# Optimization experiments

Measured on AMD Instinct MI355X. Metric: run time of the kernel, lower is better.

The kernel has to match this reference:

```python
import jax, jax.numpy as jnp
import numpy as np

E_ROUTER = 32      # routed experts with real FFNs
ZERO_E = 8         # zero-experts (identity skip)
TOP_K = 4
ROUTED_SCALE = 2.5


def setup_inputs() -> dict:
    key = jax.random.key(0)
    k1, k2, k3, k4, k5 = jax.random.split(key, 5)
    T, H, I = 2048, 1024, 512
    N = E_ROUTER + ZERO_E
    return {
        "hidden_states": jax.random.normal(k1, (T, H), jnp.float32),
        "router_w": jax.random.normal(k2, (N, H), jnp.float32) * 0.02,            # classifier weight [N, H]
        "e_score_correction_bias": jax.random.normal(k3, (N,), jnp.float32) * 0.01,
        "w13": jax.random.normal(k4, (E_ROUTER, 2 * I, H), jnp.float32) * 0.02,   # gate+up per expert
        "w2": jax.random.normal(k5, (E_ROUTER, H, I), jnp.float32) * 0.02,        # down proj per expert
    }


def reference(hidden_states, router_w, e_score_correction_bias, w13, w2):
    T, H = hidden_states.shape
    I = w2.shape[-1]

    # --- router (LongcatFlashTopkRouter) ---
    logits = hidden_states @ router_w.T                         # [T, N]
    scores = jax.nn.softmax(logits, axis=-1)
    biased = scores + e_score_correction_bias[None, :]
    _, topk_ids = jax.lax.top_k(biased, TOP_K)                  # indices chosen on biased scores
    topk_w = jnp.take_along_axis(scores, topk_ids, axis=-1) * ROUTED_SCALE  # weights from unbiased scores

    # --- zero experts: ids >= E_ROUTER contribute weight * x directly ---
    zero_mask = topk_ids >= E_ROUTER
    zero_total = jnp.sum(jnp.where(zero_mask, topk_w, 0.0), axis=-1, keepdims=True)  # [T,1]
    zero_expert_output = hidden_states * zero_total
    topk_w = jnp.where(zero_mask, 0.0, topk_w)
    topk_ids = jnp.where(zero_mask, 0, topk_ids)

    # --- combine weights per (token, expert): scatter-add of topk weights ---
    combine = jnp.zeros((T, E_ROUTER), jnp.float32).at[
        jnp.arange(T)[:, None], topk_ids
    ].add(topk_w)                                               # [T, E]

    # --- experts: swiglu FFN per expert (dense form of grouped GEMM; zero combine
    #     weights make it mathematically identical to dispatch/compute/combine) ---
    gate_up = jnp.einsum('th,eih->eti', hidden_states, w13)     # [E, T, 2I]
    gate, up = gate_up[..., :I], gate_up[..., I:]
    h = jax.nn.silu(gate) * up                                  # [E, T, I]
    expert_out = jnp.einsum('eti,ehi->eth', h, w2)              # [E, T, H]
    routed = jnp.einsum('eth,te->th', expert_out, combine)      # [T, H]

    return routed + zero_expert_output
```

## Files before the change

### kernel.cpp

```cpp
#include <hip/hip_runtime.h>
#include <math.h>

#define TT 2048
#define HH 1024
#define NE 40
#define ER 32
#define II 512
#define TOPK 4
#define RSCALE 2.5f
#define MAXW 96

typedef __bf16 bf16x8 __attribute__((ext_vector_type(8)));
typedef float f32x4 __attribute__((ext_vector_type(4)));

__global__ __launch_bounds__(256) void k_logits(const float* __restrict__ hidden,
                                                const float* __restrict__ rw,
                                                float* __restrict__ logits,
                                                int* __restrict__ cnt,
                                                int* __restrict__ cursor) {
  int tid = threadIdx.x;
  if (blockIdx.x == 0 && tid < 32) { cnt[tid] = 0; cursor[tid] = 0; }
  int lane = tid & 63;
  int t = blockIdx.x * 4 + (tid >> 6);
  const float* hrow = hidden + (size_t)t * HH;
  float4 hv[4];
  #pragma unroll
  for (int c = 0; c < 4; c++)
    hv[c] = *(const float4*)(hrow + c * 256 + lane * 4);
  float mylg = 0.f;
  for (int e = 0; e < NE; e++) {
    const float* wrow = rw + (size_t)e * HH;
    float p = 0.f;
    #pragma unroll
    for (int c = 0; c < 4; c++) {
      float4 wv = *(const float4*)(wrow + c * 256 + lane * 4);
      p += hv[c].x * wv.x + hv[c].y * wv.y + hv[c].z * wv.z + hv[c].w * wv.w;
    }
    #pragma unroll
    for (int off = 32; off; off >>= 1) p += __shfl_xor(p, off);
    if (lane == e) mylg = p;
  }
  if (lane < NE) logits[(size_t)t * NE + lane] = mylg;
}

__global__ __launch_bounds__(256) void k_route(const float* __restrict__ logits,
                                               const float* __restrict__ bias,
                                               const float* __restrict__ hidden,
                                               float* __restrict__ out,
                                               int* __restrict__ cnt,
                                               int* __restrict__ tok4_id,
                                               float* __restrict__ tok4_w,
                                               __bf16* __restrict__ hid_bf) {
  int lane = threadIdx.x & 63;
  int t = blockIdx.x * 4 + (threadIdx.x >> 6);
  float lg = (lane < NE) ? logits[(size_t)t * NE + lane] : -INFINITY;
  float m = lg;
  #pragma unroll
  for (int off = 32; off; off >>= 1) m = fmaxf(m, __shfl_xor(m, off));
  float p = (lane < NE) ? expf(lg - m) : 0.f;
  float s = p;
  #pragma unroll
  for (int off = 32; off; off >>= 1) s += __shfl_xor(s, off);
  float score = p / s;
  float v = (lane < NE) ? score + bias[lane] : -INFINITY;
  int ids[TOPK]; float wv[TOPK];
  #pragma unroll
  for (int k = 0; k < TOPK; k++) {
    float mv = v;
    int mi = (lane < NE) ? lane : 63;
    #pragma unroll
    for (int off = 32; off; off >>= 1) {
      float ov = __shfl_xor(mv, off);
      int oi = __shfl_xor(mi, off);
      if (ov > mv || (ov == mv && oi < mi)) { mv = ov; mi = oi; }
    }
    ids[k] = mi;
    wv[k] = RSCALE * __shfl(score, mi);
    if (lane == mi) v = -INFINITY;
  }
  float zt = 0.f;
  #pragma unroll
  for (int k = 0; k < TOPK; k++) if (ids[k] >= ER) zt += wv[k];
  if (lane == 0) {
    #pragma unroll
    for (int k = 0; k < TOPK; k++) {
      tok4_id[t * TOPK + k] = ids[k];
      tok4_w[t * TOPK + k] = wv[k];
      if (ids[k] < ER) atomicAdd(&cnt[ids[k]], 1);
    }
  }
  #pragma unroll
  for (int c = 0; c < 4; c++) {
    int j = c * 256 + lane * 4;
    float4 h4 = *(const float4*)(hidden + (size_t)t * HH + j);
    float4 o4 = make_float4(h4.x * zt, h4.y * zt, h4.z * zt, h4.w * zt);
    *(float4*)(out + (size_t)t * HH + j) = o4;
    union { __bf16 h[4]; uint2 u; } pk;
    pk.h[0] = (__bf16)h4.x; pk.h[1] = (__bf16)h4.y;
    pk.h[2] = (__bf16)h4.z; pk.h[3] = (__bf16)h4.w;
    *(uint2*)(hid_bf + (size_t)t * HH + j) = pk.u;
  }
}

__global__ void k_scan(const int* __restrict__ cnt, int* __restrict__ offs,
                       int* __restrict__ wl_e, int* __restrict__ wl_m0,
                       int* __restrict__ nwork) {
  int lane = threadIdx.x;
  int c = (lane < ER) ? cnt[lane] : 0;
  int ts = (c + 127) >> 7;
  int ps = c, pt = ts;
  #pragma unroll
  for (int off = 1; off < 32; off <<= 1) {
    int v1 = __shfl_up(ps, off);
    int v2 = __shfl_up(pt, off);
    if (lane >= off) { ps += v1; pt += v2; }
  }
  if (lane < ER) {
    offs[lane] = ps - c;
    int tb = pt - ts;
    for (int i = 0; i < ts; i++) { wl_e[tb + i] = lane; wl_m0[tb + i] = i * 128; }
  }
  if (lane == 31) *nwork = pt;
}

__global__ __launch_bounds__(256) void k_scatter(const int* __restrict__ tok4_id,
                                                 const float* __restrict__ tok4_w,
                                                 const int* __restrict__ offs,
                                                 int* __restrict__ cursor,
                                                 int* __restrict__ pair_tok,
                                                 float* __restrict__ pair_w) {
  int idx = blockIdx.x * 256 + threadIdx.x;
  int id = tok4_id[idx];
  if (id < ER) {
    int slot = atomicAdd(&cursor[id], 1);
    int p = offs[id] + slot;
    pair_tok[p] = idx >> 2;
    pair_w[p] = tok4_w[idx];
  }
}

__global__ __launch_bounds__(256) void k_w13(const __bf16* __restrict__ hid_bf,
                                             const float* __restrict__ w13,
                                             const int* __restrict__ cnt,
                                             const int* __restrict__ offs,
                                             const int* __restrict__ pair_tok,
                                             const int* __restrict__ wl_e,
                                             const int* __restrict__ wl_m0,
                                             const int* __restrict__ nwork,
                                             __bf16* __restrict__ h_buf) {
  int bx = blockIdx.x;
  if (bx >= *nwork) return;
  int e = wl_e[bx], m0w = wl_m0[bx];
  int M = cnt[e] - m0w; if (M > 128) M = 128;
  int base = offs[e] + m0w;
  int n0 = blockIdx.y * 64;

  __shared__ __bf16 As[128][72];
  __shared__ __bf16 Bs[128][72];
  __shared__ int tl[128];

  int tid = threadIdx.x;
  int lane = tid & 63, wid = tid >> 6;
  int wr = wid & 1, wc = wid >> 1;
  int quad = lane >> 4, rr = lane & 15;

  if (tid < 128) tl[tid] = pair_tok[base + ((tid < M) ? tid : 0)];

  const float* wg_base = w13 + (size_t)e * (2 * II) * HH + (size_t)n0 * HH;
  const float* wu_base = w13 + (size_t)e * (2 * II) * HH + (size_t)(II + n0) * HH;

  f32x4 accg[4][2] = {};
  f32x4 accu[4][2] = {};
  __syncthreads();

  for (int k0 = 0; k0 < HH; k0 += 64) {
    #pragma unroll
    for (int p = 0; p < 4; p++) {
      int s = p * 256 + tid;
      int r = s >> 3, c = (s & 7) * 8;
      *(uint4*)&As[r][c] = *(const uint4*)(hid_bf + (size_t)tl[r] * HH + k0 + c);
    }
    #pragma unroll
    for (int p = 0; p < 8; p++) {
      int s = p * 256 + tid;
      int r = s >> 4, c = (s & 15) * 4;
      const float* src = ((r < 64) ? (wg_base + (size_t)r * HH)
                                   : (wu_base + (size_t)(r - 64) * HH)) + k0 + c;
      float4 v = *(const float4*)src;
      union { __bf16 h[4]; uint2 u; } pk;
      pk.h[0] = (__bf16)v.x; pk.h[1] = (__bf16)v.y;
      pk.h[2] = (__bf16)v.z; pk.h[3] = (__bf16)v.w;
      *(uint2*)&Bs[r][c] = pk.u;
    }
    __syncthreads();
    #pragma unroll
    for (int ks = 0; ks < 2; ks++) {
      int kb = ks * 32 + quad * 8;
      bf16x8 a[4], bg[2], bu[2];
      #pragma unroll
      for (int i = 0; i < 4; i++) a[i] = *(const bf16x8*)&As[wr * 64 + i * 16 + rr][kb];
      #pragma unroll
      for (int j = 0; j < 2; j++) {
        bg[j] = *(const bf16x8*)&Bs[wc * 32 + j * 16 + rr][kb];
        bu[j] = *(const bf16x8*)&Bs[64 + wc * 32 + j * 16 + rr][kb];
      }
      #pragma unroll
      for (int i = 0; i < 4; i++)
        #pragma unroll
        for (int j = 0; j < 2; j++) {
          accg[i][j] = __builtin_amdgcn_mfma_f32_16x16x32_bf16(a[i], bg[j], accg[i][j], 0, 0, 0);
          accu[i][j] = __builtin_amdgcn_mfma_f32_16x16x32_bf16(a[i], bu[j], accu[i][j], 0, 0, 0);
        }
    }
    __syncthreads();
  }
  #pragma unroll
  for (int i = 0; i < 4; i++)
    #pragma unroll
    for (int j = 0; j < 2; j++)
      #pragma unroll
      for (int l = 0; l < 4; l++) {
        int m = wr * 64 + i * 16 + quad * 4 + l;
        if (m < M) {
          float g = accg[i][j][l], u = accu[i][j][l];
          float hv = g / (1.f + expf(-g)) * u;
          h_buf[(size_t)(base + m) * II + n0 + wc * 32 + j * 16 + rr] = (__bf16)hv;
        }
      }
}

__global__ __launch_bounds__(256) void k_w2(const __bf16* __restrict__ h_buf,
                                            const float* __restrict__ w2,
                                            const int* __restrict__ cnt,
                                            const int* __restrict__ offs,
                                            const int* __restrict__ pair_tok,
                                            const float* __restrict__ pair_w,
                                            const int* __restrict__ wl_e,
                                            const int* __restrict__ wl_m0,
                                            const int* __restrict__ nwork,
                                            float* __restrict__ out) {
  int bx = blockIdx.x;
  if (bx >= *nwork) return;
  int e = wl_e[bx], m0w = wl_m0[bx];
  int M = cnt[e] - m0w; if (M > 128) M = 128;
  int base = offs[e] + m0w;
  int h0 = blockIdx.y * 128;

  __shared__ __bf16 As[128][72];
  __shared__ __bf16 Bs[128][72];
  __shared__ int tl[128];
  __shared__ float wl[128];

  int tid = threadIdx.x;
  int lane = tid & 63, wid = tid >> 6;
  int wr = wid & 1, wc = wid >> 1;
  int quad = lane >> 4, rr = lane & 15;

  if (tid < 128) {
    int ok = tid < M;
    tl[tid] = ok ? pair_tok[base + tid] : 0;
    wl[tid] = ok ? pair_w[base + tid] : 0.f;
  }
  const __bf16* h_base = h_buf + (size_t)base * II;
  const float* w_base = w2 + (size_t)e * HH * II + (size_t)h0 * II;

  f32x4 acc[4][4] = {};
  __syncthreads();

  for (int k0 = 0; k0 < II; k0 += 64) {
    #pragma unroll
    for (int p = 0; p < 4; p++) {
      int s = p * 256 + tid;
      int r = s >> 3, c = (s & 7) * 8;
      *(uint4*)&As[r][c] = *(const uint4*)(h_base + (size_t)r * II + k0 + c);
    }
    #pragma unroll
    for (int p = 0; p < 8; p++) {
      int s = p * 256 + tid;
      int r = s >> 4, c = (s & 15) * 4;
      float4 v = *(const float4*)(w_base + (size_t)r * II + k0 + c);
      union { __bf16 h[4]; uint2 u; } pk;
      pk.h[0] = (__bf16)v.x; pk.h[1] = (__bf16)v.y;
      pk.h[2] = (__bf16)v.z; pk.h[3] = (__bf16)v.w;
      *(uint2*)&Bs[r][c] = pk.u;
    }
    __syncthreads();
    #pragma unroll
    for (int ks = 0; ks < 2; ks++) {
      int kb = ks * 32 + quad * 8;
      bf16x8 a[4], b[4];
      #pragma unroll
      for (int i = 0; i < 4; i++) a[i] = *(const bf16x8*)&As[wr * 64 + i * 16 + rr][kb];
      #pragma unroll
      for (int j = 0; j < 4; j++) b[j] = *(const bf16x8*)&Bs[wc * 64 + j * 16 + rr][kb];
      #pragma unroll
      for (int i = 0; i < 4; i++)
        #pragma unroll
        for (int j = 0; j < 4; j++)
          acc[i][j] = __builtin_amdgcn_mfma_f32_16x16x32_bf16(a[i], b[j], acc[i][j], 0, 0, 0);
    }
    __syncthreads();
  }
  #pragma unroll
  for (int i = 0; i < 4; i++)
    #pragma unroll
    for (int l = 0; l < 4; l++) {
      int m = wr * 64 + i * 16 + quad * 4 + l;
      if (m < M) {
        int t = tl[m];
        float wp = wl[m];
        #pragma unroll
        for (int j = 0; j < 4; j++)
          atomicAdd(&out[(size_t)t * HH + h0 + wc * 64 + j * 16 + rr], acc[i][j][l] * wp);
      }
    }
}

extern "C" void kernel_launch(void* const* d_in, const int* in_sizes, int n_in,
                              void* d_out, int out_size, void* d_ws, size_t ws_size,
                              hipStream_t stream) {
  const float* hidden = (const float*)d_in[0];
  const float* rw     = (const float*)d_in[1];
  const float* bias   = (const float*)d_in[2];
  const float* w13    = (const float*)d_in[3];
  const float* w2     = (const float*)d_in[4];
  float* out = (float*)d_out;

  float* ws_f = (float*)d_ws;
  float* logits = ws_f;
  int* cnt = (int*)(logits + (size_t)TT * NE + TT);
  int* offs = cnt + 32;
  int* cursor = offs + 32;
  int* tok4_id = cursor + 32;
  float* tok4_w = (float*)(tok4_id + TT * TOPK);
  int* pair_tok = (int*)(tok4_w + TT * TOPK);
  float* pair_w = (float*)(pair_tok + TT * TOPK);
  int* wl_e = (int*)(pair_w + TT * TOPK);
  int* wl_m0 = wl_e + 128;
  int* nwork = wl_m0 + 128;
  __bf16* hid_bf = (__bf16*)(nwork + 64);
  __bf16* h_buf = hid_bf + (size_t)TT * HH;

  k_logits<<<dim3(TT / 4), dim3(256), 0, stream>>>(hidden, rw, logits, cnt, cursor);
  k_route<<<dim3(TT / 4), dim3(256), 0, stream>>>(logits, bias, hidden, out,
                                                  cnt, tok4_id, tok4_w, hid_bf);
  k_scan<<<dim3(1), dim3(64), 0, stream>>>(cnt, offs, wl_e, wl_m0, nwork);
  k_scatter<<<dim3(TT * TOPK / 256), dim3(256), 0, stream>>>(tok4_id, tok4_w, offs,
                                                             cursor, pair_tok, pair_w);
  k_w13<<<dim3(MAXW, 8), dim3(256), 0, stream>>>(hid_bf, w13, cnt, offs, pair_tok,
                                                 wl_e, wl_m0, nwork, h_buf);
  k_w2<<<dim3(MAXW, 8), dim3(256), 0, stream>>>(h_buf, w2, cnt, offs, pair_tok, pair_w,
                                                wl_e, wl_m0, nwork, out);
}
```

Before: 363.1 us.

## Fuse router kernels, merge scan+scatter, retile expert GEMMs to 256-row tiles

Merges the logits and routing kernels into one, so logits no longer round-trip through memory and hidden is not reloaded. Replaces the global-atomic count, scan and scatter kernels with a single one-block kernel that counts, scans and scatters using shared-memory atomics. The expert GEMMs change from 128x128 tiles to 256-row tiles with narrower N tiles, so each expert weight tile is read once per 256 tokens rather than per 128. The tradeoff is a serial single-block scatter, larger shared memory per GEMM block (possibly lower occupancy), and fewer launch overheads.

```diff
diff --git a/kernel.cpp b/kernel.cpp
--- a/kernel.cpp
+++ b/kernel.cpp
@@ -8,56 +8,42 @@
 #define II 512
 #define TOPK 4
 #define RSCALE 2.5f
-#define MAXW 96
+#define MAXW 64
 
 typedef __bf16 bf16x8 __attribute__((ext_vector_type(8)));
 typedef float f32x4 __attribute__((ext_vector_type(4)));
 
-__global__ __launch_bounds__(256) void k_logits(const float* __restrict__ hidden,
+__global__ __launch_bounds__(256) void k_router(const float* __restrict__ hidden,
                                                 const float* __restrict__ rw,
-                                                float* __restrict__ logits,
-                                                int* __restrict__ cnt,
-                                                int* __restrict__ cursor) {
-  int tid = threadIdx.x;
-  if (blockIdx.x == 0 && tid < 32) { cnt[tid] = 0; cursor[tid] = 0; }
-  int lane = tid & 63;
-  int t = blockIdx.x * 4 + (tid >> 6);
+                                                const float* __restrict__ bias,
+                                                float* __restrict__ out,
+                                                int* __restrict__ tok4_id,
+                                                float* __restrict__ tok4_w,
+                                                __bf16* __restrict__ hid_bf) {
+  int lane = threadIdx.x & 63;
+  int t = blockIdx.x * 4 + (threadIdx.x >> 6);
   const float* hrow = hidden + (size_t)t * HH;
   float4 hv[4];
   #pragma unroll
-  for (int c = 0; c < 4; c++)
-    hv[c] = *(const float4*)(hrow + c * 256 + lane * 4);
-  float mylg = 0.f;
+  for (int c = 0; c < 4; c++) hv[c] = *(const float4*)(hrow + c * 256 + lane * 4);
+
+  float mylg = -INFINITY;
   for (int e = 0; e < NE; e++) {
     const float* wrow = rw + (size_t)e * HH;
     float p = 0.f;
     #pragma unroll
     for (int c = 0; c < 4; c++) {
-      float4 wv = *(const float4*)(wrow + c * 256 + lane * 4);
-      p += hv[c].x * wv.x + hv[c].y * wv.y + hv[c].z * wv.z + hv[c].w * wv.w;
+      float4 w4 = *(const float4*)(wrow + c * 256 + lane * 4);
+      p += hv[c].x * w4.x + hv[c].y * w4.y + hv[c].z * w4.z + hv[c].w * w4.w;
     }
     #pragma unroll
     for (int off = 32; off; off >>= 1) p += __shfl_xor(p, off);
     if (lane == e) mylg = p;
   }
-  if (lane < NE) logits[(size_t)t * NE + lane] = mylg;
-}
-
-__global__ __launch_bounds__(256) void k_route(const float* __restrict__ logits,
-                                               const float* __restrict__ bias,
-                                               const float* __restrict__ hidden,
-                                               float* __restrict__ out,
-                                               int* __restrict__ cnt,
-                                               int* __restrict__ tok4_id,
-                                               float* __restrict__ tok4_w,
-                                               __bf16* __restrict__ hid_bf) {
-  int lane = threadIdx.x & 63;
-  int t = blockIdx.x * 4 + (threadIdx.x >> 6);
-  float lg = (lane < NE) ? logits[(size_t)t * NE + lane] : -INFINITY;
-  float m = lg;
+  float m = mylg;
   #pragma unroll
   for (int off = 32; off; off >>= 1) m = fmaxf(m, __shfl_xor(m, off));
-  float p = (lane < NE) ? expf(lg - m) : 0.f;
+  float p = (lane < NE) ? expf(mylg - m) : 0.f;
   float s = p;
   #pragma unroll
   for (int off = 32; off; off >>= 1) s += __shfl_xor(s, off);
@@ -86,15 +72,14 @@
     for (int k = 0; k < TOPK; k++) {
       tok4_id[t * TOPK + k] = ids[k];
       tok4_w[t * TOPK + k] = wv[k];
-      if (ids[k] < ER) atomicAdd(&cnt[ids[k]], 1);
     }
   }
   #pragma unroll
   for (int c = 0; c < 4; c++) {
     int j = c * 256 + lane * 4;
-    float4 h4 = *(const float4*)(hidden + (size_t)t * HH + j);
-    float4 o4 = make_float4(h4.x * zt, h4.y * zt, h4.z * zt, h4.w * zt);
-    *(float4*)(out + (size_t)t * HH + j) = o4;
+    float4 h4 = hv[c];
+    *(float4*)(out + (size_t)t * HH + j) =
+        make_float4(h4.x * zt, h4.y * zt, h4.z * zt, h4.w * zt);
     union { __bf16 h[4]; uint2 u; } pk;
     pk.h[0] = (__bf16)h4.x; pk.h[1] = (__bf16)h4.y;
     pk.h[2] = (__bf16)h4.z; pk.h[3] = (__bf16)h4.w;
@@ -102,40 +87,56 @@
   }
 }
 
-__global__ void k_scan(const int* __restrict__ cnt, int* __restrict__ offs,
-                       int* __restrict__ wl_e, int* __restrict__ wl_m0,
-                       int* __restrict__ nwork) {
-  int lane = threadIdx.x;
-  int c = (lane < ER) ? cnt[lane] : 0;
-  int ts = (c + 127) >> 7;
-  int ps = c, pt = ts;
-  #pragma unroll
-  for (int off = 1; off < 32; off <<= 1) {
-    int v1 = __shfl_up(ps, off);
-    int v2 = __shfl_up(pt, off);
-    if (lane >= off) { ps += v1; pt += v2; }
-  }
-  if (lane < ER) {
-    offs[lane] = ps - c;
-    int tb = pt - ts;
-    for (int i = 0; i < ts; i++) { wl_e[tb + i] = lane; wl_m0[tb + i] = i * 128; }
-  }
-  if (lane == 31) *nwork = pt;
-}
-
-__global__ __launch_bounds__(256) void k_scatter(const int* __restrict__ tok4_id,
-                                                 const float* __restrict__ tok4_w,
-                                                 const int* __restrict__ offs,
-                                                 int* __restrict__ cursor,
-                                                 int* __restrict__ pair_tok,
-                                                 float* __restrict__ pair_w) {
-  int idx = blockIdx.x * 256 + threadIdx.x;
-  int id = tok4_id[idx];
-  if (id < ER) {
-    int slot = atomicAdd(&cursor[id], 1);
-    int p = offs[id] + slot;
-    pair_tok[p] = idx >> 2;
-    pair_w[p] = tok4_w[idx];
+__global__ __launch_bounds__(256) void k_scanscatter(const int* __restrict__ tok4_id,
+                                                     const float* __restrict__ tok4_w,
+                                                     int* __restrict__ cnt,
+                                                     int* __restrict__ offs,
+                                                     int* __restrict__ wl_e,
+                                                     int* __restrict__ wl_m0,
+                                                     int* __restrict__ nwork,
+                                                     int* __restrict__ pair_tok,
+                                                     float* __restrict__ pair_w) {
+  __shared__ int scnt[32];
+  __shared__ int scur[32];
+  int tid = threadIdx.x;
+  if (tid < 32) scnt[tid] = 0;
+  __syncthreads();
+  int ids[32]; float wv[32];
+  #pragma unroll
+  for (int i = 0; i < 32; i++) {
+    int idx = i * 256 + tid;
+    ids[i] = tok4_id[idx];
+    wv[i] = tok4_w[idx];
+    if (ids[i] < ER) atomicAdd(&scnt[ids[i]], 1);
+  }
+  __syncthreads();
+  if (tid < 64) {
+    int lane = tid;
+    int c = (lane < ER) ? scnt[lane] : 0;
+    int ts = (c + 255) >> 8;
+    int ps = c, pt = ts;
+    #pragma unroll
+    for (int off = 1; off < 32; off <<= 1) {
+      int v1 = __shfl_up(ps, off);
+      int v2 = __shfl_up(pt, off);
+      if (lane >= off) { ps += v1; pt += v2; }
+    }
+    if (lane < ER) {
+      int o = ps - c;
+      offs[lane] = o; cnt[lane] = c; scur[lane] = o;
+      int tb = pt - ts;
+      for (int i = 0; i < ts; i++) { wl_e[tb + i] = lane; wl_m0[tb + i] = i * 256; }
+    }
+    if (lane == 31) *nwork = pt;
+  }
+  __syncthreads();
+  #pragma unroll
+  for (int i = 0; i < 32; i++) {
+    if (ids[i] < ER) {
+      int pos = atomicAdd(&scur[ids[i]], 1);
+      pair_tok[pos] = (i * 256 + tid) >> 2;
+      pair_w[pos] = wv[i];
+    }
   }
 }
 
@@ -151,20 +152,19 @@
   int bx = blockIdx.x;
   if (bx >= *nwork) return;
   int e = wl_e[bx], m0w = wl_m0[bx];
-  int M = cnt[e] - m0w; if (M > 128) M = 128;
+  int M = cnt[e] - m0w; if (M > 256) M = 256;
   int base = offs[e] + m0w;
-  int n0 = blockIdx.y * 64;
-
-  __shared__ __bf16 As[128][72];
-  __shared__ __bf16 Bs[128][72];
-  __shared__ int tl[128];
+  int n0 = blockIdx.y * 32;
+
+  __shared__ __bf16 As[256][72];
+  __shared__ __bf16 Bs[64][72];
+  __shared__ int tl[256];
 
   int tid = threadIdx.x;
-  int lane = tid & 63, wid = tid >> 6;
-  int wr = wid & 1, wc = wid >> 1;
+  int lane = tid & 63, w = tid >> 6;
   int quad = lane >> 4, rr = lane & 15;
 
-  if (tid < 128) tl[tid] = pair_tok[base + ((tid < M) ? tid : 0)];
+  tl[tid] = pair_tok[base + ((tid < M) ? tid : 0)];
 
   const float* wg_base = w13 + (size_t)e * (2 * II) * HH + (size_t)n0 * HH;
   const float* wu_base = w13 + (size_t)e * (2 * II) * HH + (size_t)(II + n0) * HH;
@@ -175,17 +175,17 @@
 
   for (int k0 = 0; k0 < HH; k0 += 64) {
     #pragma unroll
-    for (int p = 0; p < 4; p++) {
+    for (int p = 0; p < 8; p++) {
       int s = p * 256 + tid;
       int r = s >> 3, c = (s & 7) * 8;
       *(uint4*)&As[r][c] = *(const uint4*)(hid_bf + (size_t)tl[r] * HH + k0 + c);
     }
     #pragma unroll
-    for (int p = 0; p < 8; p++) {
+    for (int p = 0; p < 4; p++) {
       int s = p * 256 + tid;
       int r = s >> 4, c = (s & 15) * 4;
-      const float* src = ((r < 64) ? (wg_base + (size_t)r * HH)
-                                   : (wu_base + (size_t)(r - 64) * HH)) + k0 + c;
+      const float* src = ((r < 32) ? (wg_base + (size_t)r * HH)
+                                   : (wu_base + (size_t)(r - 32) * HH)) + k0 + c;
       float4 v = *(const float4*)src;
       union { __bf16 h[4]; uint2 u; } pk;
       pk.h[0] = (__bf16)v.x; pk.h[1] = (__bf16)v.y;
@@ -198,11 +198,11 @@
       int kb = ks * 32 + quad * 8;
       bf16x8 a[4], bg[2], bu[2];
       #pragma unroll
-      for (int i = 0; i < 4; i++) a[i] = *(const bf16x8*)&As[wr * 64 + i * 16 + rr][kb];
+      for (int i = 0; i < 4; i++) a[i] = *(const bf16x8*)&As[w * 64 + i * 16 + rr][kb];
       #pragma unroll
       for (int j = 0; j < 2; j++) {
-        bg[j] = *(const bf16x8*)&Bs[wc * 32 + j * 16 + rr][kb];
-        bu[j] = *(const bf16x8*)&Bs[64 + wc * 32 + j * 16 + rr][kb];
+        bg[j] = *(const bf16x8*)&Bs[j * 16 + rr][kb];
+        bu[j] = *(const bf16x8*)&Bs[32 + j * 16 + rr][kb];
       }
       #pragma unroll
       for (int i = 0; i < 4; i++)
@@ -220,11 +220,11 @@
     for (int j = 0; j < 2; j++)
       #pragma unroll
       for (int l = 0; l < 4; l++) {
-        int m = wr * 64 + i * 16 + quad * 4 + l;
+        int m = w * 64 + i * 16 + quad * 4 + l;
         if (m < M) {
           float g = accg[i][j][l], u = accu[i][j][l];
           float hv = g / (1.f + expf(-g)) * u;
-          h_buf[(size_t)(base + m) * II + n0 + wc * 32 + j * 16 + rr] = (__bf16)hv;
+          h_buf[(size_t)(base + m) * II + n0 + j * 16 + rr] = (__bf16)hv;
         }
       }
 }
@@ -242,21 +242,20 @@
   int bx = blockIdx.x;
   if (bx >= *nwork) return;
   int e = wl_e[bx], m0w = wl_m0[bx];
-  int M = cnt[e] - m0w; if (M > 128) M = 128;
+  int M = cnt[e] - m0w; if (M > 256) M = 256;
   int base = offs[e] + m0w;
-  int h0 = blockIdx.y * 128;
-
-  __shared__ __bf16 As[128][72];
-  __shared__ __bf16 Bs[128][72];
-  __shared__ int tl[128];
-  __shared__ float wl[128];
+  int h0 = blockIdx.y * 64;
+
+  __shared__ __bf16 As[256][72];
+  __shared__ __bf16 Bs[64][72];
+  __shared__ int tl[256];
+  __shared__ float wl[256];
 
   int tid = threadIdx.x;
-  int lane = tid & 63, wid = tid >> 6;
-  int wr = wid & 1, wc = wid >> 1;
+  int lane = tid & 63, w = tid >> 6;
   int quad = lane >> 4, rr = lane & 15;
 
-  if (tid < 128) {
+  {
     int ok = tid < M;
     tl[tid] = ok ? pair_tok[base + tid] : 0;
     wl[tid] = ok ? pair_w[base + tid] : 0.f;
@@ -269,13 +268,13 @@
 
   for (int k0 = 0; k0 < II; k0 += 64) {
     #pragma unroll
-    for (int p = 0; p < 4; p++) {
+    for (int p = 0; p < 8; p++) {
       int s = p * 256 + tid;
       int r = s >> 3, c = (s & 7) * 8;
       *(uint4*)&As[r][c] = *(const uint4*)(h_base + (size_t)r * II + k0 + c);
     }
     #pragma unroll
-    for (int p = 0; p < 8; p++) {
+    for (int p = 0; p < 4; p++) {
       int s = p * 256 + tid;
       int r = s >> 4, c = (s & 15) * 4;
       float4 v = *(const float4*)(w_base + (size_t)r * II + k0 + c);
@@ -290,9 +289,9 @@
       int kb = ks * 32 + quad * 8;
       bf16x8 a[4], b[4];
       #pragma unroll
-      for (int i = 0; i < 4; i++) a[i] = *(const bf16x8*)&As[wr * 64 + i * 16 + rr][kb];
-      #pragma unroll
-      for (int j = 0; j < 4; j++) b[j] = *(const bf16x8*)&Bs[wc * 64 + j * 16 + rr][kb];
+      for (int i = 0; i < 4; i++) a[i] = *(const bf16x8*)&As[w * 64 + i * 16 + rr][kb];
+      #pragma unroll
+      for (int j = 0; j < 4; j++) b[j] = *(const bf16x8*)&Bs[j * 16 + rr][kb];
       #pragma unroll
       for (int i = 0; i < 4; i++)
         #pragma unroll
@@ -305,13 +304,13 @@
   for (int i = 0; i < 4; i++)
     #pragma unroll
     for (int l = 0; l < 4; l++) {
-      int m = wr * 64 + i * 16 + quad * 4 + l;
+      int m = w * 64 + i * 16 + quad * 4 + l;
       if (m < M) {
         int t = tl[m];
         float wp = wl[m];
         #pragma unroll
         for (int j = 0; j < 4; j++)
-          atomicAdd(&out[(size_t)t * HH + h0 + wc * 64 + j * 16 + rr], acc[i][j][l] * wp);
+          atomicAdd(&out[(size_t)t * HH + h0 + j * 16 + rr], acc[i][j][l] * wp);
       }
     }
 }
@@ -326,29 +325,25 @@
   const float* w2     = (const float*)d_in[4];
   float* out = (float*)d_out;
 
-  float* ws_f = (float*)d_ws;
-  float* logits = ws_f;
-  int* cnt = (int*)(logits + (size_t)TT * NE + TT);
-  int* offs = cnt + 32;
-  int* cursor = offs + 32;
-  int* tok4_id = cursor + 32;
+  int* ws_i = (int*)d_ws;
+  int* tok4_id = ws_i;
   float* tok4_w = (float*)(tok4_id + TT * TOPK);
   int* pair_tok = (int*)(tok4_w + TT * TOPK);
   float* pair_w = (float*)(pair_tok + TT * TOPK);
-  int* wl_e = (int*)(pair_w + TT * TOPK);
-  int* wl_m0 = wl_e + 128;
-  int* nwork = wl_m0 + 128;
+  int* cnt = (int*)(pair_w + TT * TOPK);
+  int* offs = cnt + 32;
+  int* wl_e = offs + 32;
+  int* wl_m0 = wl_e + 64;
+  int* nwork = wl_m0 + 64;
   __bf16* hid_bf = (__bf16*)(nwork + 64);
   __bf16* h_buf = hid_bf + (size_t)TT * HH;
 
-  k_logits<<<dim3(TT / 4), dim3(256), 0, stream>>>(hidden, rw, logits, cnt, cursor);
-  k_route<<<dim3(TT / 4), dim3(256), 0, stream>>>(logits, bias, hidden, out,
-                                                  cnt, tok4_id, tok4_w, hid_bf);
-  k_scan<<<dim3(1), dim3(64), 0, stream>>>(cnt, offs, wl_e, wl_m0, nwork);
-  k_scatter<<<dim3(TT * TOPK / 256), dim3(256), 0, stream>>>(tok4_id, tok4_w, offs,
-                                                             cursor, pair_tok, pair_w);
-  k_w13<<<dim3(MAXW, 8), dim3(256), 0, stream>>>(hid_bf, w13, cnt, offs, pair_tok,
-                                                 wl_e, wl_m0, nwork, h_buf);
-  k_w2<<<dim3(MAXW, 8), dim3(256), 0, stream>>>(h_buf, w2, cnt, offs, pair_tok, pair_w,
-                                                wl_e, wl_m0, nwork, out);
-}
+  k_router<<<dim3(TT / 4), dim3(256), 0, stream>>>(hidden, rw, bias, out,
+                                                   tok4_id, tok4_w, hid_bf);
+  k_scanscatter<<<dim3(1), dim3(256), 0, stream>>>(tok4_id, tok4_w, cnt, offs,
+                                                   wl_e, wl_m0, nwork, pair_tok, pair_w);
+  k_w13<<<dim3(MAXW, 16), dim3(256), 0, stream>>>(hid_bf, w13, cnt, offs, pair_tok,
+                                                  wl_e, wl_m0, nwork, h_buf);
+  k_w2<<<dim3(MAXW, 16), dim3(256), 0, stream>>>(h_buf, w2, cnt, offs, pair_tok, pair_w,
+                                                 wl_e, wl_m0, nwork, out);
+}
```

Result: faster. 341.9 us (-5.8%).
